# Performance work log

Hardware: AMD Instinct MI355X
Metric: run time of the kernel (lower is better)

Reference implementation:

```python
import jax, jax.numpy as jnp
import numpy as np

FP8_MAX = 448.0  # e4m3 max
SCALE_MARGIN = 0.8


def _fp8_quant_dequant(t, scale):
    # scaled value is <= 448*0.8 by construction, so no saturation/overflow
    q = (t / scale).astype(jnp.float8_e4m3fn)
    return q.astype(jnp.float32) * scale


def setup_inputs() -> dict:
    key = jax.random.key(0)
    k1, k2 = jax.random.split(key)
    B, S, D_IN, D_OUT = 4, 2048, 2048, 2048
    x = jax.random.normal(k1, (B, S, D_IN), dtype=jnp.float32)
    weight = jax.random.normal(k2, (D_OUT, D_IN), dtype=jnp.float32)
    bias = jnp.zeros((D_OUT,), dtype=jnp.float32)
    return {"x": x, "weight": weight, "bias": bias}


def reference(x, weight, bias):
    # Shared FP8ScalingManager: amax history = [amax_x] for x, then [amax_x, amax_w] for w.
    amax_x = jnp.max(jnp.abs(x))
    amax_w = jnp.max(jnp.abs(weight))
    x_scale = amax_x / (FP8_MAX * SCALE_MARGIN)
    w_scale = jnp.maximum(amax_x, amax_w) / (FP8_MAX * SCALE_MARGIN)  # history max
    x_scale = jax.lax.stop_gradient(x_scale)  # .item() detaches in torch
    w_scale = jax.lax.stop_gradient(w_scale)
    # quantize to fp8 e4m3, dequantize, scaled matmul (math of torch._scaled_mm)
    x_dq = _fp8_quant_dequant(x, x_scale)      # [B,S,Din]
    w_dq = _fp8_quant_dequant(weight, w_scale)  # [Dout,Din]
    out = jnp.einsum('bsd,od->bso', x_dq, w_dq)  # [B,S,Dout]
    return out + bias
```

## Files before the change

kernel.cpp:

```cpp
#include <hip/hip_runtime.h>
#include <stdint.h>

typedef float v4f __attribute__((ext_vector_type(4)));
typedef int v8i __attribute__((ext_vector_type(8)));

#define FP8_DENOM 358.4f


__device__ __forceinline__ unsigned pack4_fp8(float a, float b, float c, float d) {
  int v = 0;
  v = __builtin_amdgcn_cvt_pk_fp8_f32(a, b, v, false);
  v = __builtin_amdgcn_cvt_pk_fp8_f32(c, d, v, true);
  return (unsigned)v;
}

__device__ __forceinline__ void gload_lds16(const void* g, void* l) {
  __builtin_amdgcn_global_load_lds(
      (const __attribute__((address_space(1))) uint32_t*)(uintptr_t)g,
      (__attribute__((address_space(3))) uint32_t*)(uint32_t)(uintptr_t)l,
      16, 0, 0);
}


__global__ void __launch_bounds__(256) amax_part(const float4* __restrict__ x,
                                                 const float4* __restrict__ w,
                                                 unsigned* __restrict__ amax) {
  const int b = blockIdx.x, t = threadIdx.x;
  const int isw = (b >= 1024) ? 1 : 0;
  const float4* p = isw ? w : x;
  const long base = (long)(isw ? (b - 1024) : b) * 4096;
  float m0 = 0.f, m1 = 0.f, m2 = 0.f, m3 = 0.f;
#pragma unroll
  for (int j = 0; j < 4; ++j) {
    float4 v0 = p[base + (j * 4 + 0) * 256 + t];
    float4 v1 = p[base + (j * 4 + 1) * 256 + t];
    float4 v2 = p[base + (j * 4 + 2) * 256 + t];
    float4 v3 = p[base + (j * 4 + 3) * 256 + t];
    m0 = fmaxf(m0, fmaxf(fmaxf(fabsf(v0.x), fabsf(v0.y)), fmaxf(fabsf(v0.z), fabsf(v0.w))));
    m1 = fmaxf(m1, fmaxf(fmaxf(fabsf(v1.x), fabsf(v1.y)), fmaxf(fabsf(v1.z), fabsf(v1.w))));
    m2 = fmaxf(m2, fmaxf(fmaxf(fabsf(v2.x), fabsf(v2.y)), fmaxf(fabsf(v2.z), fabsf(v2.w))));
    m3 = fmaxf(m3, fmaxf(fmaxf(fabsf(v3.x), fabsf(v3.y)), fmaxf(fabsf(v3.z), fabsf(v3.w))));
  }
  float m = fmaxf(fmaxf(m0, m1), fmaxf(m2, m3));
#pragma unroll
  for (int off = 32; off > 0; off >>= 1)
    m = fmaxf(m, __shfl_down(m, off, 64));
  __shared__ float red[4];
  const int lane = t & 63, wvid = t >> 6;
  if (lane == 0) red[wvid] = m;
  __syncthreads();
  if (t == 0)
    atomicMax(amax + isw,
              __float_as_uint(fmaxf(fmaxf(red[0], red[1]), fmaxf(red[2], red[3]))));
}


__global__ void __launch_bounds__(256) quant2_kernel(
    const float4* __restrict__ x, unsigned* __restrict__ xq,
    const float4* __restrict__ w, unsigned* __restrict__ wq,
    const unsigned* __restrict__ amax) {
  const int t = threadIdx.x;
  const int isw = ((int)blockIdx.x >= 4096) ? 1 : 0;
  const float ax = __uint_as_float(amax[0]);
  const float aw = __uint_as_float(amax[1]);
  const float s = (isw ? fmaxf(ax, aw) : ax) / FP8_DENOM;
  const float rs = 1.0f / s;
  const float4* in = isw ? w : x;
  unsigned* outq = isw ? wq : xq;
  const long base = (long)(isw ? ((int)blockIdx.x - 4096) : (int)blockIdx.x) * 1024;
#pragma unroll
  for (int j = 0; j < 4; ++j) {
    float4 v = in[base + j * 256 + t];
    outq[base + j * 256 + t] = pack4_fp8(v.x * rs, v.y * rs, v.z * rs, v.w * rs);
  }
}


__global__ void __launch_bounds__(512, 2) gemm_mx(
    const uint8_t* __restrict__ Aq, const uint8_t* __restrict__ Bq,
    const float* __restrict__ bias, float* __restrict__ out,
    const unsigned* __restrict__ amax) {
  constexpr int K = 2048, N = 2048, BK = 128, ITERS = K / BK;
  __shared__ alignas(16) uint8_t sA[2][256 * BK];
  __shared__ alignas(16) uint8_t sB[2][256 * BK];

  const int tid = threadIdx.x;
  const int lane = tid & 63;
  const int wid = tid >> 6;
  const int wy = wid >> 2, wx = wid & 3;

  const int orig = (int)blockIdx.y * (int)gridDim.x + (int)blockIdx.x;
  const int wg = (orig & 7) * 32 + (orig >> 3);
  const long tileM = (long)(wg >> 3) * 256;
  const long tileN = (long)(wg & 7) * 256;

  v4f acc[8][4];
#pragma unroll
  for (int i = 0; i < 8; ++i)
#pragma unroll
    for (int j = 0; j < 4; ++j) acc[i][j] = (v4f)(0.f);

  const int srow = tid >> 3;
  const int schunk = (tid & 7) ^ (srow & 7);
  const uint8_t* gA = Aq + (tileM + srow) * K + schunk * 16;
  const uint8_t* gB = Bq + (tileN + srow) * K + schunk * 16;

  const int q = lane >> 4;
  const int mrow = lane & 15;
  const int sw = mrow & 7;
  const int aoff0 = (wy * 128 + mrow) * BK + 16 * ((2 * q) ^ sw);
  const int aoff1 = (wy * 128 + mrow) * BK + 16 * ((2 * q + 1) ^ sw);
  const int boff0 = (wx * 64 + mrow) * BK + 16 * ((2 * q) ^ sw);
  const int boff1 = (wx * 64 + mrow) * BK + 16 * ((2 * q + 1) ^ sw);

  auto stage = [&](int buf, int k0) {
#pragma unroll
    for (int s = 0; s < 4; ++s) {
      gload_lds16(gA + (long)s * 64 * K + k0, &sA[buf][s * 8192 + tid * 16]);
      gload_lds16(gB + (long)s * 64 * K + k0, &sB[buf][s * 8192 + tid * 16]);
    }
  };

  stage(0, 0);
  stage(1, BK);

  union Frag { v8i v; uint4 h[2]; };

  for (int it = 0; it < ITERS; ++it) {
    const int cur = it & 1;

    if (it + 1 < ITERS)
      asm volatile("s_waitcnt vmcnt(8)" ::: "memory");
    else
      asm volatile("s_waitcnt vmcnt(0)" ::: "memory");
    __builtin_amdgcn_s_barrier();
    __builtin_amdgcn_sched_barrier(0);

    const uint8_t* bufA = sA[cur];
    const uint8_t* bufB = sB[cur];

    Frag a[8], b[4];
#pragma unroll
    for (int j = 0; j < 4; ++j) {
      b[j].h[0] = *(const uint4*)(bufB + boff0 + j * 16 * BK);
      b[j].h[1] = *(const uint4*)(bufB + boff1 + j * 16 * BK);
    }
#pragma unroll
    for (int i = 0; i < 8; ++i) {
      a[i].h[0] = *(const uint4*)(bufA + aoff0 + i * 16 * BK);
      a[i].h[1] = *(const uint4*)(bufA + aoff1 + i * 16 * BK);
    }

    __builtin_amdgcn_s_setprio(1);
#pragma unroll
    for (int i = 0; i < 8; ++i)
#pragma unroll
      for (int j = 0; j < 4; ++j)
        acc[i][j] = __builtin_amdgcn_mfma_scale_f32_16x16x128_f8f6f4(
            a[i].v, b[j].v, acc[i][j],  0,  0,
             0, 0x7F7F7F7F,  0, 0x7F7F7F7F);
    __builtin_amdgcn_s_setprio(0);

    if (it + 2 < ITERS) {
      asm volatile("s_waitcnt lgkmcnt(0)" ::: "memory");
      __builtin_amdgcn_s_barrier();
      stage(cur, (it + 2) * BK);
    }
  }

  const float ax = __uint_as_float(amax[0]);
  const float aw = __uint_as_float(amax[1]);
  const float scale = (ax / FP8_DENOM) * (fmaxf(ax, aw) / FP8_DENOM);
#pragma unroll
  for (int j = 0; j < 4; ++j) {
    const long col = tileN + wx * 64 + j * 16 + mrow;
    const float bv = bias[col];
#pragma unroll
    for (int i = 0; i < 8; ++i) {
      const long row = tileM + wy * 128 + i * 16 + q * 4;
#pragma unroll
      for (int r = 0; r < 4; ++r)
        out[(row + r) * N + col] = acc[i][j][r] * scale + bv;
    }
  }
}


extern "C" void kernel_launch(void* const* d_in, const int* in_sizes, int n_in,
                              void* d_out, int out_size, void* d_ws, size_t ws_size,
                              hipStream_t stream) {
  const float* x = (const float*)d_in[0];
  const float* w = (const float*)d_in[1];
  const float* bias = (const float*)d_in[2];
  float* out = (float*)d_out;

  const int M = 8192, N = 2048, K = 2048;
  const long nx = (long)M * K;

  unsigned* amax = (unsigned*)d_ws;
  uint8_t* xq = (uint8_t*)d_ws + 8192;
  uint8_t* wq = xq + nx;

  hipMemsetAsync(amax, 0, 8, stream);
  amax_part<<<1280, 256, 0, stream>>>((const float4*)x, (const float4*)w, amax);
  quant2_kernel<<<5120, 256, 0, stream>>>((const float4*)x, (unsigned*)xq,
                                          (const float4*)w, (unsigned*)wq, amax);
  gemm_mx<<<dim3(N / 256, M / 256), 512, 0, stream>>>(xq, wq, bias, out, amax);
}
```

Before: 179.4 us.

## Shrink GEMM tile to 128x128 with 32x32x64 scaled MFMA and 4 waves

The FP8 GEMM moves from 256x256 tiles with 8 waves and 16x16x128 MFMAs to 128x128 tiles with 4 waves, BK=64 and 32x32x64 scaled MFMAs, so each wave computes a 64x64 sub-tile. The LDS swizzle, the staging layout and the block remap are redone for the new shape, and the launch becomes 1024 blocks of 256 threads. The aim is more blocks per CU and fewer accumulator registers, which should improve occupancy and latency hiding. The cost is lower data reuse per tile, roughly twice the global and LDS traffic per FLOP, and twice as many k-iterations with a barrier each.

```diff
diff --git a/kernel.cpp b/kernel.cpp
--- a/kernel.cpp
+++ b/kernel.cpp
@@ -2,6 +2,7 @@
 #include <stdint.h>
 
 typedef float v4f __attribute__((ext_vector_type(4)));
+typedef float v16f __attribute__((ext_vector_type(16)));
 typedef int v8i __attribute__((ext_vector_type(8)));
 
 #define FP8_DENOM 358.4f
@@ -76,48 +77,50 @@
 }
 
 
-__global__ void __launch_bounds__(512, 2) gemm_mx(
+__global__ void __launch_bounds__(256, 4) gemm_mx(
     const uint8_t* __restrict__ Aq, const uint8_t* __restrict__ Bq,
     const float* __restrict__ bias, float* __restrict__ out,
     const unsigned* __restrict__ amax) {
-  constexpr int K = 2048, N = 2048, BK = 128, ITERS = K / BK;
-  __shared__ alignas(16) uint8_t sA[2][256 * BK];
-  __shared__ alignas(16) uint8_t sB[2][256 * BK];
+  constexpr int K = 2048, N = 2048, BK = 64, ITERS = K / BK;
+  __shared__ alignas(16) uint8_t sA[2][128 * BK];
+  __shared__ alignas(16) uint8_t sB[2][128 * BK];
 
   const int tid = threadIdx.x;
   const int lane = tid & 63;
   const int wid = tid >> 6;
-  const int wy = wid >> 2, wx = wid & 3;
+  const int wy = wid >> 1, wx = wid & 1;
 
   const int orig = (int)blockIdx.y * (int)gridDim.x + (int)blockIdx.x;
-  const int wg = (orig & 7) * 32 + (orig >> 3);
-  const long tileM = (long)(wg >> 3) * 256;
-  const long tileN = (long)(wg & 7) * 256;
-
-  v4f acc[8][4];
-#pragma unroll
-  for (int i = 0; i < 8; ++i)
-#pragma unroll
-    for (int j = 0; j < 4; ++j) acc[i][j] = (v4f)(0.f);
-
-  const int srow = tid >> 3;
-  const int schunk = (tid & 7) ^ (srow & 7);
-  const uint8_t* gA = Aq + (tileM + srow) * K + schunk * 16;
-  const uint8_t* gB = Bq + (tileN + srow) * K + schunk * 16;
-
-  const int q = lane >> 4;
-  const int mrow = lane & 15;
-  const int sw = mrow & 7;
-  const int aoff0 = (wy * 128 + mrow) * BK + 16 * ((2 * q) ^ sw);
-  const int aoff1 = (wy * 128 + mrow) * BK + 16 * ((2 * q + 1) ^ sw);
-  const int boff0 = (wx * 64 + mrow) * BK + 16 * ((2 * q) ^ sw);
-  const int boff1 = (wx * 64 + mrow) * BK + 16 * ((2 * q + 1) ^ sw);
+  const int wg = (orig & 7) * 128 + (orig >> 3);
+  const long tileM = (long)(wg >> 4) * 128;
+  const long tileN = (long)(wg & 15) * 128;
+
+  v16f acc[2][2];
+#pragma unroll
+  for (int i = 0; i < 2; ++i)
+#pragma unroll
+    for (int j = 0; j < 2; ++j) acc[i][j] = (v16f)(0.f);
+
+  const int clog = (tid & 3) ^ ((tid >> 3) & 3);
+  const uint8_t* gA = Aq + (tileM + (tid >> 2)) * K + clog * 16;
+  const uint8_t* gB = Bq + (tileN + (tid >> 2)) * K + clog * 16;
+
+  const int r = lane & 31, q = lane >> 5;
+  const int sw2 = (r >> 1) & 3;
+  int aoff[2][2], boff[2][2];
+#pragma unroll
+  for (int ti = 0; ti < 2; ++ti)
+#pragma unroll
+    for (int cb = 0; cb < 2; ++cb) {
+      aoff[ti][cb] = (wy * 64 + ti * 32 + r) * BK + 16 * (((q << 1) | cb) ^ sw2);
+      boff[ti][cb] = (wx * 64 + ti * 32 + r) * BK + 16 * (((q << 1) | cb) ^ sw2);
+    }
 
   auto stage = [&](int buf, int k0) {
 #pragma unroll
-    for (int s = 0; s < 4; ++s) {
-      gload_lds16(gA + (long)s * 64 * K + k0, &sA[buf][s * 8192 + tid * 16]);
-      gload_lds16(gB + (long)s * 64 * K + k0, &sB[buf][s * 8192 + tid * 16]);
+    for (int s = 0; s < 2; ++s) {
+      gload_lds16(gA + (long)s * 64 * K + k0, &sA[buf][s * 4096 + tid * 16]);
+      gload_lds16(gB + (long)s * 64 * K + k0, &sB[buf][s * 4096 + tid * 16]);
     }
   };
 
@@ -130,7 +133,7 @@
     const int cur = it & 1;
 
     if (it + 1 < ITERS)
-      asm volatile("s_waitcnt vmcnt(8)" ::: "memory");
+      asm volatile("s_waitcnt vmcnt(4)" ::: "memory");
     else
       asm volatile("s_waitcnt vmcnt(0)" ::: "memory");
     __builtin_amdgcn_s_barrier();
@@ -139,25 +142,22 @@
     const uint8_t* bufA = sA[cur];
     const uint8_t* bufB = sB[cur];
 
-    Frag a[8], b[4];
-#pragma unroll
-    for (int j = 0; j < 4; ++j) {
-      b[j].h[0] = *(const uint4*)(bufB + boff0 + j * 16 * BK);
-      b[j].h[1] = *(const uint4*)(bufB + boff1 + j * 16 * BK);
-    }
-#pragma unroll
-    for (int i = 0; i < 8; ++i) {
-      a[i].h[0] = *(const uint4*)(bufA + aoff0 + i * 16 * BK);
-      a[i].h[1] = *(const uint4*)(bufA + aoff1 + i * 16 * BK);
+    Frag a[2], b[2];
+#pragma unroll
+    for (int ti = 0; ti < 2; ++ti) {
+      b[ti].h[0] = *(const uint4*)(bufB + boff[ti][0]);
+      b[ti].h[1] = *(const uint4*)(bufB + boff[ti][1]);
+      a[ti].h[0] = *(const uint4*)(bufA + aoff[ti][0]);
+      a[ti].h[1] = *(const uint4*)(bufA + aoff[ti][1]);
     }
 
     __builtin_amdgcn_s_setprio(1);
 #pragma unroll
-    for (int i = 0; i < 8; ++i)
-#pragma unroll
-      for (int j = 0; j < 4; ++j)
-        acc[i][j] = __builtin_amdgcn_mfma_scale_f32_16x16x128_f8f6f4(
-            a[i].v, b[j].v, acc[i][j],  0,  0,
+    for (int ti = 0; ti < 2; ++ti)
+#pragma unroll
+      for (int tj = 0; tj < 2; ++tj)
+        acc[ti][tj] = __builtin_amdgcn_mfma_scale_f32_32x32x64_f8f6f4(
+            a[ti].v, b[tj].v, acc[ti][tj],  0,  0,
              0, 0x7F7F7F7F,  0, 0x7F7F7F7F);
     __builtin_amdgcn_s_setprio(0);
 
@@ -172,15 +172,17 @@
   const float aw = __uint_as_float(amax[1]);
   const float scale = (ax / FP8_DENOM) * (fmaxf(ax, aw) / FP8_DENOM);
 #pragma unroll
-  for (int j = 0; j < 4; ++j) {
-    const long col = tileN + wx * 64 + j * 16 + mrow;
+  for (int tj = 0; tj < 2; ++tj) {
+    const long col = tileN + wx * 64 + tj * 32 + r;
     const float bv = bias[col];
 #pragma unroll
-    for (int i = 0; i < 8; ++i) {
-      const long row = tileM + wy * 128 + i * 16 + q * 4;
-#pragma unroll
-      for (int r = 0; r < 4; ++r)
-        out[(row + r) * N + col] = acc[i][j][r] * scale + bv;
+    for (int ti = 0; ti < 2; ++ti) {
+      const long rowbase = tileM + wy * 64 + ti * 32 + 4 * q;
+#pragma unroll
+      for (int g = 0; g < 4; ++g)
+#pragma unroll
+        for (int rr = 0; rr < 4; ++rr)
+          out[(rowbase + 8 * g + rr) * N + col] = acc[ti][tj][g * 4 + rr] * scale + bv;
     }
   }
 }
@@ -205,5 +207,5 @@
   amax_part<<<1280, 256, 0, stream>>>((const float4*)x, (const float4*)w, amax);
   quant2_kernel<<<5120, 256, 0, stream>>>((const float4*)x, (unsigned*)xq,
                                           (const float4*)w, (unsigned*)wq, amax);
-  gemm_mx<<<dim3(N / 256, M / 256), 512, 0, stream>>>(xq, wq, bias, out, amax);
-}
+  gemm_mx<<<dim3(N / 128, M / 128), 256, 0, stream>>>(xq, wq, bias, out, amax);
+}
```

After: 179.7 us. No clear change (+0.2%).

## Software-pipeline GEMM main loop with ping-pong register fragments and interleaved LDS reads

Applied to the files above, without the earlier changes.

Restructures the fp8 MFMA main loop so LDS fragment loads for the next pair of A rows are issued while the current MFMAs run, using alternating register fragment sets and double-buffered B fragments. The loop is unrolled by two over the LDS buffers. Global-to-LDS prefetch now goes one tile ahead instead of two. This aims to hide LDS read latency behind matrix-core work, at the cost of many extra barriers per tile and a shallower global prefetch that may expose memory latency.

```diff
diff --git a/kernel.cpp b/kernel.cpp
--- a/kernel.cpp
+++ b/kernel.cpp
@@ -121,51 +121,88 @@
     }
   };
 
+  union Frag { v8i v; uint4 h[2]; };
+  Frag aE[2], aO[2], bC[4], bN[4];
+
+#define LD_A2(bufA, d, r0i)                                          \
+  do {                                                               \
+    d[0].h[0] = *(const uint4*)((bufA) + aoff0 + (r0i + 0) * 16 * BK); \
+    d[0].h[1] = *(const uint4*)((bufA) + aoff1 + (r0i + 0) * 16 * BK); \
+    d[1].h[0] = *(const uint4*)((bufA) + aoff0 + (r0i + 1) * 16 * BK); \
+    d[1].h[1] = *(const uint4*)((bufA) + aoff1 + (r0i + 1) * 16 * BK); \
+  } while (0)
+
+#define LD_B4(bufB, d)                                               \
+  do {                                                               \
+    d[0].h[0] = *(const uint4*)((bufB) + boff0 + 0 * 16 * BK);       \
+    d[0].h[1] = *(const uint4*)((bufB) + boff1 + 0 * 16 * BK);       \
+    d[1].h[0] = *(const uint4*)((bufB) + boff0 + 1 * 16 * BK);       \
+    d[1].h[1] = *(const uint4*)((bufB) + boff1 + 1 * 16 * BK);       \
+    d[2].h[0] = *(const uint4*)((bufB) + boff0 + 2 * 16 * BK);       \
+    d[2].h[1] = *(const uint4*)((bufB) + boff1 + 2 * 16 * BK);       \
+    d[3].h[0] = *(const uint4*)((bufB) + boff0 + 3 * 16 * BK);       \
+    d[3].h[1] = *(const uint4*)((bufB) + boff1 + 3 * 16 * BK);       \
+  } while (0)
+
+#define MFMA2(r0i, aa, bb)                                           \
+  do {                                                               \
+    __builtin_amdgcn_s_setprio(1);                                   \
+    _Pragma("unroll") for (int j = 0; j < 4; ++j)                    \
+        acc[r0i + 0][j] = __builtin_amdgcn_mfma_scale_f32_16x16x128_f8f6f4( \
+            aa[0].v, bb[j].v, acc[r0i + 0][j], 0, 0, 0, 0x7F7F7F7F, 0, 0x7F7F7F7F); \
+    _Pragma("unroll") for (int j = 0; j < 4; ++j)                    \
+        acc[r0i + 1][j] = __builtin_amdgcn_mfma_scale_f32_16x16x128_f8f6f4( \
+            aa[1].v, bb[j].v, acc[r0i + 1][j], 0, 0, 0, 0x7F7F7F7F, 0, 0x7F7F7F7F); \
+    __builtin_amdgcn_s_setprio(0);                                   \
+  } while (0)
+
+#define BAR()                          \
+  do {                                 \
+    __builtin_amdgcn_s_barrier();      \
+    __builtin_amdgcn_sched_barrier(0); \
+  } while (0)
+
+#define TILE_BODY(P, u, BC, BN)                                      \
+  do {                                                               \
+    const uint8_t* bA = sA[P];                                       \
+    const bool pf = (u) + 1 < ITERS;                                 \
+                                                            \
+    if (pf) stage((P) ^ 1, ((u) + 1) * BK);                          \
+    LD_A2(bA, aO, 2);                                                \
+    BAR();                                                           \
+    MFMA2(0, aE, BC);                                                \
+    BAR();                                                           \
+                                                            \
+    LD_A2(bA, aE, 4);                                                \
+    BAR();                                                           \
+    MFMA2(2, aO, BC);                                                \
+    BAR();                                                           \
+                                                            \
+    LD_A2(bA, aO, 6);                                                \
+    BAR();                                                           \
+    MFMA2(4, aE, BC);                                                \
+    BAR();                                                           \
+     \
+    asm volatile("s_waitcnt vmcnt(0)" ::: "memory");                 \
+    BAR();                                                           \
+    if (pf) {                                                        \
+      LD_A2(sA[(P) ^ 1], aE, 0);                                     \
+      LD_B4(sB[(P) ^ 1], BN);                                        \
+    }                                                                \
+    MFMA2(6, aO, BC);                                                \
+    BAR();                                                           \
+  } while (0)
+
   stage(0, 0);
-  stage(1, BK);
-
-  union Frag { v8i v; uint4 h[2]; };
-
-  for (int it = 0; it < ITERS; ++it) {
-    const int cur = it & 1;
-
-    if (it + 1 < ITERS)
-      asm volatile("s_waitcnt vmcnt(8)" ::: "memory");
-    else
-      asm volatile("s_waitcnt vmcnt(0)" ::: "memory");
-    __builtin_amdgcn_s_barrier();
-    __builtin_amdgcn_sched_barrier(0);
-
-    const uint8_t* bufA = sA[cur];
-    const uint8_t* bufB = sB[cur];
-
-    Frag a[8], b[4];
-#pragma unroll
-    for (int j = 0; j < 4; ++j) {
-      b[j].h[0] = *(const uint4*)(bufB + boff0 + j * 16 * BK);
-      b[j].h[1] = *(const uint4*)(bufB + boff1 + j * 16 * BK);
-    }
-#pragma unroll
-    for (int i = 0; i < 8; ++i) {
-      a[i].h[0] = *(const uint4*)(bufA + aoff0 + i * 16 * BK);
-      a[i].h[1] = *(const uint4*)(bufA + aoff1 + i * 16 * BK);
-    }
-
-    __builtin_amdgcn_s_setprio(1);
-#pragma unroll
-    for (int i = 0; i < 8; ++i)
-#pragma unroll
-      for (int j = 0; j < 4; ++j)
-        acc[i][j] = __builtin_amdgcn_mfma_scale_f32_16x16x128_f8f6f4(
-            a[i].v, b[j].v, acc[i][j],  0,  0,
-             0, 0x7F7F7F7F,  0, 0x7F7F7F7F);
-    __builtin_amdgcn_s_setprio(0);
-
-    if (it + 2 < ITERS) {
-      asm volatile("s_waitcnt lgkmcnt(0)" ::: "memory");
-      __builtin_amdgcn_s_barrier();
-      stage(cur, (it + 2) * BK);
-    }
+  asm volatile("s_waitcnt vmcnt(0)" ::: "memory");
+  __builtin_amdgcn_s_barrier();
+  __builtin_amdgcn_sched_barrier(0);
+  LD_B4(sB[0], bC);
+  LD_A2(sA[0], aE, 0);
+
+  for (int u = 0; u < ITERS; u += 2) {
+    TILE_BODY(0, u, bC, bN);
+    TILE_BODY(1, u + 1, bN, bC);
   }
 
   const float ax = __uint_as_float(amax[0]);
@@ -183,6 +220,11 @@
         out[(row + r) * N + col] = acc[i][j][r] * scale + bv;
     }
   }
+#undef TILE_BODY
+#undef BAR
+#undef MFMA2
+#undef LD_B4
+#undef LD_A2
 }
 
 
```

Result: slower. 387.1 us (+115.8%).
